# Optimization experiments

Measured on AMD Instinct MI355X. Metric: run time of the kernel, lower is better.

The kernel has to match this reference:

```python
import jax, jax.numpy as jnp
import numpy as np

HIDDEN = 1024
HEADS = 16
HEAD_DIM = HIDDEN // HEADS


def setup_inputs() -> dict:
    key = jax.random.key(0)
    k_x, k_wq, k_bq, k_wo, k_bo = jax.random.split(key, 5)
    x = jax.random.normal(k_x, (2, 2048, HIDDEN), dtype=jnp.float32)
    s = 1.0 / np.sqrt(HIDDEN)
    W_qkv = jax.random.uniform(k_wq, (HIDDEN, 3 * HIDDEN), jnp.float32, -s, s)
    b_qkv = jax.random.uniform(k_bq, (3 * HIDDEN,), jnp.float32, -s, s)
    W_out = jax.random.uniform(k_wo, (HIDDEN, HIDDEN), jnp.float32, -s, s)
    b_out = jax.random.uniform(k_bo, (HIDDEN,), jnp.float32, -s, s)
    return {"x": x, "W_qkv": W_qkv, "b_qkv": b_qkv, "W_out": W_out, "b_out": b_out}


def reference(x, W_qkv, b_qkv, W_out, b_out):
    B, S, D = x.shape
    qkv = x @ W_qkv + b_qkv                       # [B,S,3D]
    qkv = qkv.reshape(B, S, 3, HEADS, HEAD_DIM)
    qkv = jnp.transpose(qkv, (2, 0, 3, 1, 4))     # [3,B,H,S,Dh]
    q, k, v = qkv[0], qkv[1], qkv[2]
    scores = jnp.einsum("bhsd,bhtd->bhst", q, k) / np.sqrt(HEAD_DIM)
    attn = jax.nn.softmax(scores, axis=-1)        # [B,H,S,S]
    out = jnp.einsum("bhst,bhtd->bhsd", attn, v)  # [B,H,S,Dh]
    out = jnp.transpose(out, (0, 2, 1, 3)).reshape(B, S, D)
    return out @ W_out + b_out
```

## Files before the change

kernel.cpp:

```cpp
#include <hip/hip_runtime.h>
#include <hip/hip_bf16.h>

typedef short short8 __attribute__((ext_vector_type(8)));
typedef float float4_ __attribute__((ext_vector_type(4)));
typedef unsigned short ushort_t;
typedef unsigned int uint32_t_;
typedef uint32_t_ uint2v __attribute__((ext_vector_type(2)));
typedef uint32_t_ uint4v __attribute__((ext_vector_type(4)));

#define SCL 0.1803368801111f

__device__ __forceinline__ ushort_t f2bf(float f) {
    uint32_t_ u = __builtin_bit_cast(uint32_t_, f);
    u = (u + 0x7fffu + ((u >> 16) & 1u)) >> 16;
    return (ushort_t)u;
}

__device__ __forceinline__ uint32_t_ pack_bf16(float a, float b) {
    uint32_t_ ua = __builtin_bit_cast(uint32_t_, a) + 0x8000u;
    uint32_t_ ub = __builtin_bit_cast(uint32_t_, b) + 0x8000u;
    return __builtin_amdgcn_perm(ub, ua, 0x07060302);
}

__device__ __forceinline__ uint32_t_ cvt_pk_bf16(float lo, float hi) {
    uint32_t_ r;
    asm("v_cvt_pk_bf16_f32 %0, %1, %2" : "=v"(r) : "v"(lo), "v"(hi));
    return r;
}

#define MFMA32(a, b, c) __builtin_amdgcn_mfma_f32_16x16x32_bf16(a, b, c, 0, 0, 0)

#define GLD_LDS16(g, l) __builtin_amdgcn_global_load_lds( \
    (const __attribute__((address_space(1))) void*)(g),   \
    (__attribute__((address_space(3))) void*)(l), 16, 0, 0)

__global__ __launch_bounds__(256)
void prep_k(const float* __restrict__ x, ushort_t* __restrict__ x_bf,
            const float* __restrict__ Wqkv, ushort_t* __restrict__ WqkvT,
            const float* __restrict__ Wout, ushort_t* __restrict__ WoutT) {
    __shared__ float tile[32][33];
    const int id = blockIdx.x;
    const int tid = threadIdx.x;
    if (id < 2048) {
        int i = (id * 256 + tid) * 8;
        float4 v0 = *(const float4*)(x + i);
        float4 v1 = *(const float4*)(x + i + 4);
        uint4v d;
        d.x = (uint32_t_)f2bf(v0.x) | ((uint32_t_)f2bf(v0.y) << 16);
        d.y = (uint32_t_)f2bf(v0.z) | ((uint32_t_)f2bf(v0.w) << 16);
        d.z = (uint32_t_)f2bf(v1.x) | ((uint32_t_)f2bf(v1.y) << 16);
        d.w = (uint32_t_)f2bf(v1.z) | ((uint32_t_)f2bf(v1.w) << 16);
        *(uint4v*)(x_bf + i) = d;
        return;
    }
    const float* in;
    ushort_t* out;
    int N, K, n0, k0;
    if (id < 5120) {
        int t = id - 2048;
        in = Wqkv; out = WqkvT; N = 3072; K = 1024;
        n0 = (t % 96) * 32; k0 = (t / 96) * 32;
    } else {
        int t = id - 5120;
        in = Wout; out = WoutT; N = 1024; K = 1024;
        n0 = (t & 31) * 32; k0 = (t >> 5) * 32;
    }
    int tx = tid & 31, ty = tid >> 5;
    #pragma unroll
    for (int i = 0; i < 32; i += 8)
        tile[ty + i][tx] = in[(size_t)(k0 + ty + i) * N + n0 + tx];
    __syncthreads();
    #pragma unroll
    for (int i = 0; i < 32; i += 8)
        out[(size_t)(n0 + ty + i) * K + k0 + tx] = f2bf(tile[tx][ty + i]);
}

template <int TN, bool QKV_EPI>
__global__ __launch_bounds__(256, TN == 128 ? 3 : 4)
void gemm_dbuf_k(const ushort_t* __restrict__ A, const ushort_t* __restrict__ Bt,
                 const float* __restrict__ bias, void* __restrict__ C,
                 ushort_t* __restrict__ Vt_out, int M, int N, int K) {
    constexpr int NB   = TN / 32;
    constexpr int SETB = 8192 + TN * 64;
    __shared__ char smem[2 * SETB];
    const int tid  = threadIdx.x;
    const int nwg = gridDim.x * gridDim.y;
    const int id  = blockIdx.y * gridDim.x + blockIdx.x;
    const int sid = (id & 7) * (nwg >> 3) + (id >> 3);
    const int m0  = (sid / gridDim.x) * 128;
    const int n0  = (sid % gridDim.x) * TN;
    const int w    = tid >> 6;
    const int lane = tid & 63;
    const int wm   = (w >> 1) * 64;
    const int wn   = (w & 1) * (TN / 2);
    const int quad = lane >> 4;
    const int l16  = lane & 15;

    const int sr = 16 * w + (lane >> 2);
    const int sc = ((lane & 3) ^ ((sr >> 1) & 3)) * 8;
    const ushort_t* ag0 = A  + (size_t)(m0 + sr) * K + sc;
    const ushort_t* ag1 = A  + (size_t)(m0 + sr + 64) * K + sc;
    const ushort_t* bg0 = Bt + (size_t)(n0 + sr) * K + sc;
    const ushort_t* bg1 = Bt + (size_t)(n0 + sr + 64) * K + sc;
    char* sA = smem + 1024 * w;
    char* sB = smem + 8192 + 1024 * w;

    int aoff[4], boff[NB];
    #pragma unroll
    for (int i = 0; i < 4; i++) {
        int row = wm + i * 16 + l16;
        aoff[i] = row * 64 + ((quad ^ ((row >> 1) & 3)) * 16);
    }
    #pragma unroll
    for (int i = 0; i < NB; i++) {
        int row = wn + i * 16 + l16;
        boff[i] = 8192 + row * 64 + ((quad ^ ((row >> 1) & 3)) * 16);
    }

    float4_ acc[4][NB] = {};
    const int NIT = K >> 5;

    GLD_LDS16(ag0, sA);
    GLD_LDS16(ag1, sA + 4096);
    GLD_LDS16(bg0, sB);
    if (TN == 128) GLD_LDS16(bg1, sB + 4096);

    for (int it = 0; it < NIT; ++it) {
        __syncthreads();
        if (it + 1 < NIT) {
            const int nk = (it + 1) * 32;
            char* dA = sA + ((it + 1) & 1) * SETB;
            char* dB = sB + ((it + 1) & 1) * SETB;
            GLD_LDS16(ag0 + nk, dA);
            GLD_LDS16(ag1 + nk, dA + 4096);
            GLD_LDS16(bg0 + nk, dB);
            if (TN == 128) GLD_LDS16(bg1 + nk, dB + 4096);
        }
        const char* base = smem + (it & 1) * SETB;
        short8 af[4], bf[NB];
        #pragma unroll
        for (int i = 0; i < 4; i++)  af[i] = *(const short8*)(base + aoff[i]);
        #pragma unroll
        for (int i = 0; i < NB; i++) bf[i] = *(const short8*)(base + boff[i]);
        #pragma unroll
        for (int mi = 0; mi < 4; mi++)
            #pragma unroll
            for (int ni = 0; ni < NB; ni++)
                acc[mi][ni] = MFMA32(af[mi], bf[ni], acc[mi][ni]);
    }

    #pragma unroll
    for (int mi = 0; mi < 4; mi++) {
        int row = m0 + wm + mi * 16 + quad * 4;
        #pragma unroll
        for (int ni = 0; ni < NB; ni++) {
            int col = n0 + wn + ni * 16 + l16;
            float bb = bias[col];
            if (QKV_EPI) {
                if (col < 2048) {
                    float sc2 = (col < 1024) ? SCL : 1.0f;
                    #pragma unroll
                    for (int r = 0; r < 4; r++)
                        ((ushort_t*)C)[(size_t)(row + r) * 2048 + col] =
                            f2bf((acc[mi][ni][r] + bb) * sc2);
                } else {
                    int s0v  = row & 2047;
                    int spos = (s0v & ~31) | (quad << 3) | ((mi & 1) << 2);
                    size_t vrow = (size_t)((row >> 11) * 1024 + (col - 2048));
                    float v0 = acc[mi][ni][0] + bb, v1 = acc[mi][ni][1] + bb;
                    float v2 = acc[mi][ni][2] + bb, v3 = acc[mi][ni][3] + bb;
                    uint2v pk;
                    pk.x = pack_bf16(v0, v1);
                    pk.y = pack_bf16(v2, v3);
                    *(uint2v*)(Vt_out + vrow * 2048 + spos) = pk;
                }
            } else {
                #pragma unroll
                for (int r = 0; r < 4; r++)
                    ((float*)C)[(size_t)(row + r) * N + col] = acc[mi][ni][r] + bb;
            }
        }
    }
}

__global__ __launch_bounds__(512, 4)
void flash_attn_k(const ushort_t* __restrict__ qk, const ushort_t* __restrict__ vt,
                  ushort_t* __restrict__ out) {
    __shared__ char smem[49152];
    const int bh = blockIdx.x;
    const int b  = bh >> 4, h = bh & 15;
    const int q0 = blockIdx.y * 128;
    const int tid  = threadIdx.x;
    const int w    = tid >> 6;
    const int lane = tid & 63;
    const int quad = lane >> 4;
    const int l16  = lane & 15;
    const int qh   = w >> 1;
    const int kh   = w & 1;
    const size_t tok0 = (size_t)b * 2048;
    const int hq = h * 64;

    const int s7  = lane & 7;
    const int rk  = 8 * w + (lane >> 3);
    const int ck  = (s7 ^ ((rk >> 1) & 7)) * 8;
    const int rq0 = 16 * w + (lane >> 3), rq1 = rq0 + 8;
    const int cq0 = (s7 ^ ((rq0 >> 1) & 7)) * 8;
    const int cq1 = (s7 ^ ((rq1 >> 1) & 7)) * 8;
    const ushort_t* qg0 = qk + (tok0 + q0 + rq0) * 2048 + hq + cq0;
    const ushort_t* qg1 = qk + (tok0 + q0 + rq1) * 2048 + hq + cq1;
    const ushort_t* kg  = qk + (tok0 + rk) * 2048 + 1024 + hq + ck;
    const ushort_t* vg  = vt + (size_t)(bh * 64 + rk) * 2048 + ck;
    char* stK = smem + 1024 * w;
    char* stV = smem + 8192 + 1024 * w;
    char* stQ = smem + 32768 + 2048 * w;

    GLD_LDS16(qg0, stQ);
    GLD_LDS16(qg1, stQ + 1024);
    GLD_LDS16(kg, stK);
    GLD_LDS16(vg, stV);
    __syncthreads();

    const int sw = (l16 >> 1) & 7;
    short8 qf[2][2];
    #pragma unroll
    for (int sub = 0; sub < 2; sub++)
        #pragma unroll
        for (int kk = 0; kk < 2; kk++) {
            int row = qh * 32 + sub * 16 + l16;
            qf[sub][kk] = *(const short8*)(smem + 32768 + row * 128 +
                                           (((kk * 4 + quad) ^ sw) * 16));
        }

    int koff[2][2], voff[4];
    #pragma unroll
    for (int mi = 0; mi < 2; mi++)
        #pragma unroll
        for (int kk = 0; kk < 2; kk++) {
            int row = kh * 32 + mi * 16 + l16;
            koff[mi][kk] = row * 128 + (((kk * 4 + quad) ^ sw) * 16);
        }
    #pragma unroll
    for (int di = 0; di < 4; di++) {
        int row = di * 16 + l16;
        voff[di] = 8192 + row * 128 + (((kh * 4 + quad) ^ sw) * 16);
    }

    float4_ ot[2][4] = {};
    float lsum[2] = {0.f, 0.f};
    short8 vprev[4];
    short8 bpprev[2];

    const ushort_t* kp = kg + (size_t)64 * 2048;
    const ushort_t* vp = vg + 64;

    {
        __syncthreads();
        GLD_LDS16(kp, stK + 16384);
        GLD_LDS16(vp, stV + 16384);
        kp += (size_t)64 * 2048;
        vp += 64;
        const char* base = smem;
        float4_ st[2][2];
        #pragma unroll
        for (int mi = 0; mi < 2; mi++) {
            short8 kf0 = *(const short8*)(base + koff[mi][0]);
            short8 kf1 = *(const short8*)(base + koff[mi][1]);
            #pragma unroll
            for (int sub = 0; sub < 2; sub++) {
                float4_ z = {0.f, 0.f, 0.f, 0.f};
                z = MFMA32(kf0, qf[sub][0], z);
                z = MFMA32(kf1, qf[sub][1], z);
                st[mi][sub] = z;
            }
        }
        #pragma unroll
        for (int di = 0; di < 4; di++)
            vprev[di] = *(const short8*)(base + voff[di]);
        #pragma unroll
        for (int sub = 0; sub < 2; sub++) {
            uint4v u;
            #pragma unroll
            for (int mi = 0; mi < 2; mi++) {
                float p0 = __builtin_amdgcn_exp2f(st[mi][sub][0]);
                float p1 = __builtin_amdgcn_exp2f(st[mi][sub][1]);
                float p2 = __builtin_amdgcn_exp2f(st[mi][sub][2]);
                float p3 = __builtin_amdgcn_exp2f(st[mi][sub][3]);
                lsum[sub] += (p0 + p1) + (p2 + p3);
                if (mi == 0) { u.x = cvt_pk_bf16(p0, p1); u.y = cvt_pk_bf16(p2, p3); }
                else         { u.z = cvt_pk_bf16(p0, p1); u.w = cvt_pk_bf16(p2, p3); }
            }
            bpprev[sub] = __builtin_bit_cast(short8, u);
        }
    }

    for (int kt = 64; kt < 2048; kt += 64) {
        __syncthreads();
        const int set = (kt >> 6) & 1;
        if (kt + 64 < 2048) {
            const int nb = (set ^ 1) * 16384;
            GLD_LDS16(kp, stK + nb);
            GLD_LDS16(vp, stV + nb);
            kp += (size_t)64 * 2048;
            vp += 64;
        }
        const char* base = smem + set * 16384;

        float4_ st[2][2];
        #pragma unroll
        for (int mi = 0; mi < 2; mi++) {
            short8 kf0 = *(const short8*)(base + koff[mi][0]);
            short8 kf1 = *(const short8*)(base + koff[mi][1]);
            #pragma unroll
            for (int sub = 0; sub < 2; sub++) {
                float4_ z = {0.f, 0.f, 0.f, 0.f};
                z = MFMA32(kf0, qf[sub][0], z);
                z = MFMA32(kf1, qf[sub][1], z);
                st[mi][sub] = z;
            }
        }

        #pragma unroll
        for (int di = 0; di < 4; di++)
            #pragma unroll
            for (int sub = 0; sub < 2; sub++)
                ot[sub][di] = MFMA32(vprev[di], bpprev[sub], ot[sub][di]);

        #pragma unroll
        for (int di = 0; di < 4; di++)
            vprev[di] = *(const short8*)(base + voff[di]);

        #pragma unroll
        for (int sub = 0; sub < 2; sub++) {
            uint4v u;
            #pragma unroll
            for (int mi = 0; mi < 2; mi++) {
                float p0 = __builtin_amdgcn_exp2f(st[mi][sub][0]);
                float p1 = __builtin_amdgcn_exp2f(st[mi][sub][1]);
                float p2 = __builtin_amdgcn_exp2f(st[mi][sub][2]);
                float p3 = __builtin_amdgcn_exp2f(st[mi][sub][3]);
                lsum[sub] += (p0 + p1) + (p2 + p3);
                if (mi == 0) { u.x = cvt_pk_bf16(p0, p1); u.y = cvt_pk_bf16(p2, p3); }
                else         { u.z = cvt_pk_bf16(p0, p1); u.w = cvt_pk_bf16(p2, p3); }
            }
            bpprev[sub] = __builtin_bit_cast(short8, u);
        }
    }

    #pragma unroll
    for (int di = 0; di < 4; di++)
        #pragma unroll
        for (int sub = 0; sub < 2; sub++)
            ot[sub][di] = MFMA32(vprev[di], bpprev[sub], ot[sub][di]);

    #pragma unroll
    for (int sub = 0; sub < 2; sub++) {
        float t = lsum[sub];
        t += __shfl_xor(t, 16, 64);
        t += __shfl_xor(t, 32, 64);
        lsum[sub] = t;
    }

    float* Obuf = (float*)smem;
    float* lbuf = (float*)(smem + 34816);
    __syncthreads();
    #pragma unroll
    for (int sub = 0; sub < 2; sub++)
        lbuf[(qh * 32 + sub * 16 + l16) * 2 + kh] = lsum[sub];
    if (kh == 1) {
        #pragma unroll
        for (int sub = 0; sub < 2; sub++)
            #pragma unroll
            for (int di = 0; di < 4; di++)
                *(float4_*)&Obuf[(qh * 32 + sub * 16 + l16) * 68 + di * 16 + quad * 4] = ot[sub][di];
    }
    __syncthreads();
    if (kh == 0) {
        #pragma unroll
        for (int sub = 0; sub < 2; sub++)
            #pragma unroll
            for (int di = 0; di < 4; di++) {
                float4_* p = (float4_*)&Obuf[(qh * 32 + sub * 16 + l16) * 68 + di * 16 + quad * 4];
                *p = *p + ot[sub][di];
            }
    }
    __syncthreads();

    {
        int q  = tid >> 2;
        int ds = (tid & 3) * 16;
        float linv = 1.0f / (lbuf[q * 2] + lbuf[q * 2 + 1]);
        const float* ob = &Obuf[q * 68 + ds];
        float4_ v0 = *(const float4_*)(ob);
        float4_ v1 = *(const float4_*)(ob + 4);
        float4_ v2 = *(const float4_*)(ob + 8);
        float4_ v3 = *(const float4_*)(ob + 12);
        uint4v d0, d1;
        d0.x = pack_bf16(v0[0] * linv, v0[1] * linv);
        d0.y = pack_bf16(v0[2] * linv, v0[3] * linv);
        d0.z = pack_bf16(v1[0] * linv, v1[1] * linv);
        d0.w = pack_bf16(v1[2] * linv, v1[3] * linv);
        d1.x = pack_bf16(v2[0] * linv, v2[1] * linv);
        d1.y = pack_bf16(v2[2] * linv, v2[3] * linv);
        d1.z = pack_bf16(v3[0] * linv, v3[1] * linv);
        d1.w = pack_bf16(v3[2] * linv, v3[3] * linv);
        ushort_t* dst = out + (tok0 + q0 + (size_t)q) * 1024 + hq + ds;
        *(uint4v*)(dst)     = d0;
        *(uint4v*)(dst + 8) = d1;
    }
}

extern "C" void kernel_launch(void* const* d_in, const int* in_sizes, int n_in,
                              void* d_out, int out_size, void* d_ws, size_t ws_size,
                              hipStream_t stream) {
    const float* x    = (const float*)d_in[0];
    const float* Wqkv = (const float*)d_in[1];
    const float* bqkv = (const float*)d_in[2];
    const float* Wout = (const float*)d_in[3];
    const float* bout = (const float*)d_in[4];
    float* out = (float*)d_out;

    char* ws = (char*)d_ws;
    ushort_t* x_bf    = (ushort_t*)(ws);
    ushort_t* WqkvT   = (ushort_t*)(ws + 8388608);
    ushort_t* WoutT   = (ushort_t*)(ws + 14680064);
    ushort_t* qk_bf   = (ushort_t*)(ws + 16777216);
    ushort_t* vt_bf   = (ushort_t*)(ws + 33554432);
    ushort_t* attn_bf = (ushort_t*)(ws + 41943040);

    prep_k<<<6144, 256, 0, stream>>>(x, x_bf, Wqkv, WqkvT, Wout, WoutT);

    gemm_dbuf_k<128, true><<<dim3(24, 32), 256, 0, stream>>>(
        x_bf, WqkvT, bqkv, (void*)qk_bf, vt_bf, 4096, 3072, 1024);

    flash_attn_k<<<dim3(32, 16), 512, 0, stream>>>(qk_bf, vt_bf, attn_bf);

    gemm_dbuf_k<128, false><<<dim3(8, 32), 256, 0, stream>>>(
        attn_bf, WoutT, bout, (void*)out, nullptr, 4096, 1024, 1024);
}
```

Before: 172.6 us.

## Replace QKV GEMM with 256x256-tile 8-wave double-buffered kernel

Adds a dedicated QKV projection kernel that uses 256x256 output tiles with 512 threads, 128KB of LDS double buffering via direct global-to-LDS loads, and MFMA phases split by barriers with raised priority. The larger tile is meant to raise arithmetic intensity and cut global and LDS traffic per flop compared with the 128x128 generic kernel. In exchange the grid shrinks to 192 workgroups with high LDS use, so fewer than one wave of workgroups per CU and lower occupancy may hurt latency hiding. The epilogue keeps the same Q scaling and V-transpose layout.

New measurement: 177.9 us. 1.03x slower.

```diff
diff --git a/kernel.cpp b/kernel.cpp
--- a/kernel.cpp
+++ b/kernel.cpp
@@ -73,6 +73,136 @@
     #pragma unroll
     for (int i = 0; i < 32; i += 8)
         out[(size_t)(n0 + ty + i) * K + k0 + tx] = f2bf(tile[tx][ty + i]);
+}
+
+__global__ __launch_bounds__(512, 2)
+void gemm_qkv8p_k(const ushort_t* __restrict__ A, const ushort_t* __restrict__ Bt,
+                  const float* __restrict__ bias, ushort_t* __restrict__ qk,
+                  ushort_t* __restrict__ Vt_out) {
+    constexpr int K   = 1024;
+    constexpr int NIT = K / 64;
+    __shared__ char smem[131072];
+    const int tid  = threadIdx.x;
+    const int nwg  = gridDim.x * gridDim.y;
+    const int id   = blockIdx.y * gridDim.x + blockIdx.x;
+    const int sid  = (id & 7) * (nwg >> 3) + (id >> 3);
+    const int m0   = (sid / gridDim.x) * 256;
+    const int n0   = (sid % gridDim.x) * 256;
+    const int w    = tid >> 6;
+    const int lane = tid & 63;
+    const int quad = lane >> 4;
+    const int l16  = lane & 15;
+    const int wr   = w >> 2;
+    const int wc   = w & 3;
+
+    const int srow = w * 8 + (lane >> 3);
+    const int scol = ((lane & 7) ^ (lane >> 3)) * 8;
+    const ushort_t* ag[4];
+    const ushort_t* bg[4];
+    #pragma unroll
+    for (int j = 0; j < 4; j++) {
+        ag[j] = A  + (size_t)(m0 + j * 64 + srow) * K + scol;
+        bg[j] = Bt + (size_t)(n0 + j * 64 + srow) * K + scol;
+    }
+
+    const int sz0  = ((quad)     ^ (l16 & 7)) * 16;
+    const int sz1  = ((4 + quad) ^ (l16 & 7)) * 16;
+    const int aco0 = wr * 16384 + l16 * 128 + sz0;
+    const int aco1 = wr * 16384 + l16 * 128 + sz1;
+    const int bco0 = 32768 + wc * 8192 + l16 * 128 + sz0;
+    const int bco1 = 32768 + wc * 8192 + l16 * 128 + sz1;
+
+    float4_ acc[8][4] = {};
+
+    #pragma unroll
+    for (int j = 0; j < 4; j++) {
+        GLD_LDS16(ag[j], smem + 1024 * w + 8192 * j);
+        GLD_LDS16(bg[j], smem + 32768 + 1024 * w + 8192 * j);
+        ag[j] += 64; bg[j] += 64;
+    }
+    #pragma unroll
+    for (int j = 0; j < 4; j++) {
+        GLD_LDS16(ag[j], smem + 65536 + 1024 * w + 8192 * j);
+        GLD_LDS16(bg[j], smem + 65536 + 32768 + 1024 * w + 8192 * j);
+        ag[j] += 64; bg[j] += 64;
+    }
+    asm volatile("s_waitcnt vmcnt(8)" ::: "memory");
+    __builtin_amdgcn_s_barrier();
+
+    for (int kt = 0; kt < NIT; ++kt) {
+        const char* buf = smem + (kt & 1) * 65536;
+        short8 bf[4][2];
+        #pragma unroll
+        for (int p = 0; p < 4; ++p) {
+            short8 af[2][2];
+            if (p == 0) {
+                #pragma unroll
+                for (int ni = 0; ni < 4; ni++) {
+                    bf[ni][0] = *(const short8*)(buf + bco0 + ni * 2048);
+                    bf[ni][1] = *(const short8*)(buf + bco1 + ni * 2048);
+                }
+            }
+            #pragma unroll
+            for (int m2 = 0; m2 < 2; m2++) {
+                af[m2][0] = *(const short8*)(buf + aco0 + (p * 2 + m2) * 2048);
+                af[m2][1] = *(const short8*)(buf + aco1 + (p * 2 + m2) * 2048);
+            }
+            __builtin_amdgcn_s_barrier();
+            asm volatile("s_waitcnt lgkmcnt(0)" ::: "memory");
+            __builtin_amdgcn_sched_barrier(0);
+            __builtin_amdgcn_s_setprio(1);
+            #pragma unroll
+            for (int m2 = 0; m2 < 2; m2++)
+                #pragma unroll
+                for (int ni = 0; ni < 4; ni++) {
+                    acc[p * 2 + m2][ni] = MFMA32(af[m2][0], bf[ni][0], acc[p * 2 + m2][ni]);
+                    acc[p * 2 + m2][ni] = MFMA32(af[m2][1], bf[ni][1], acc[p * 2 + m2][ni]);
+                }
+            __builtin_amdgcn_s_setprio(0);
+            __builtin_amdgcn_s_barrier();
+        }
+        if (kt < NIT - 2) {
+            char* dst = smem + (kt & 1) * 65536;
+            #pragma unroll
+            for (int j = 0; j < 4; j++) {
+                GLD_LDS16(ag[j], dst + 1024 * w + 8192 * j);
+                GLD_LDS16(bg[j], dst + 32768 + 1024 * w + 8192 * j);
+                ag[j] += 64; bg[j] += 64;
+            }
+            asm volatile("s_waitcnt vmcnt(8)" ::: "memory");
+            __builtin_amdgcn_s_barrier();
+        } else if (kt == NIT - 2) {
+            asm volatile("s_waitcnt vmcnt(0)" ::: "memory");
+            __builtin_amdgcn_s_barrier();
+        }
+    }
+
+    #pragma unroll
+    for (int mi = 0; mi < 8; mi++) {
+        int row = m0 + wr * 128 + mi * 16 + quad * 4;
+        #pragma unroll
+        for (int ni = 0; ni < 4; ni++) {
+            int col = n0 + wc * 64 + ni * 16 + l16;
+            float bb = bias[col];
+            if (col < 2048) {
+                float sc2 = (col < 1024) ? SCL : 1.0f;
+                #pragma unroll
+                for (int r = 0; r < 4; r++)
+                    qk[(size_t)(row + r) * 2048 + col] =
+                        f2bf((acc[mi][ni][r] + bb) * sc2);
+            } else {
+                int s0v  = row & 2047;
+                int spos = (s0v & ~31) | (quad << 3) | ((mi & 1) << 2);
+                size_t vrow = (size_t)((row >> 11) * 1024 + (col - 2048));
+                float v0 = acc[mi][ni][0] + bb, v1 = acc[mi][ni][1] + bb;
+                float v2 = acc[mi][ni][2] + bb, v3 = acc[mi][ni][3] + bb;
+                uint2v pk;
+                pk.x = pack_bf16(v0, v1);
+                pk.y = pack_bf16(v2, v3);
+                *(uint2v*)(Vt_out + vrow * 2048 + spos) = pk;
+            }
+        }
+    }
 }
 
 template <int TN, bool QKV_EPI>
@@ -429,8 +559,7 @@
 
     prep_k<<<6144, 256, 0, stream>>>(x, x_bf, Wqkv, WqkvT, Wout, WoutT);
 
-    gemm_dbuf_k<128, true><<<dim3(24, 32), 256, 0, stream>>>(
-        x_bf, WqkvT, bqkv, (void*)qk_bf, vt_bf, 4096, 3072, 1024);
+    gemm_qkv8p_k<<<dim3(12, 16), 512, 0, stream>>>(x_bf, WqkvT, bqkv, qk_bf, vt_bf);
 
     flash_attn_k<<<dim3(32, 16), 512, 0, stream>>>(qk_bf, vt_bf, attn_bf);
 
```
